# Optimization experiments

Measured on AMD Instinct MI355X. Metric: run time of the kernel, lower is better.

The kernel has to match this reference:

```python
import jax, jax.numpy as jnp
import numpy as np

N = 512          # octave output grid resolution per cube side
M = 256          # input octave resolution
FACTOR = 0.5     # 2 ** (-factor), factor = 1
EPS = 1e-12


def make_cube_faces(n):
    # two triangles per quad on each of the 6 n x n side grids
    idx = np.arange(n * n).reshape(n, n)
    a = idx[:-1, :-1].ravel(); b = idx[:-1, 1:].ravel()
    c = idx[1:, :-1].ravel(); d = idx[1:, 1:].ravel()
    tris = np.concatenate([np.stack([a, b, c], 1), np.stack([b, d, c], 1)], 0)
    faces = np.concatenate([tris + s * n * n for s in range(6)], 0)
    return jnp.asarray(faces, jnp.int32)  # [F, 3]


def to_stacked(t):
    # [1, 6*m*m, 3] -> [6, 3, m, m]
    m = int(round((t.shape[1] // 6) ** 0.5))
    return t.reshape(6, m, m, 3).transpose(0, 3, 1, 2)


def to_vertices(s):
    # [6, 3, m, m] -> [1, 6*m*m, 3]
    return s.transpose(0, 2, 3, 1).reshape(1, -1, 3)


def resize_bilinear_ac(t, n):
    # bilinear, align_corners=True, square input [.., m, m] -> [.., n, n]
    m = t.shape[-1]
    coords = jnp.linspace(0.0, m - 1.0, n)
    i0 = jnp.clip(jnp.floor(coords).astype(jnp.int32), 0, m - 1)
    i1 = jnp.minimum(i0 + 1, m - 1)
    w = (coords - i0).astype(t.dtype)
    t = t[..., i0, :] * (1.0 - w)[:, None] + t[..., i1, :] * w[:, None]
    t = t[..., :, i0] * (1.0 - w) + t[..., :, i1] * w
    return t


def compute_face_normals(vert, faces):
    v = vert[0]                                  # [V, 3]
    v0, v1, v2 = v[faces[:, 0]], v[faces[:, 1]], v[faces[:, 2]]
    fn = jnp.cross(v1 - v0, v2 - v0)             # [F, 3]
    nrm = jnp.linalg.norm(fn, axis=-1, keepdims=True)
    return fn / jnp.maximum(nrm, EPS)


def compute_vertex_normals(vert, faces, face_normals):
    V = vert.shape[1]
    flat_idx = faces.reshape(-1)                          # [3F] f0v0,f0v1,f0v2,...
    rep = jnp.repeat(face_normals, 3, axis=0)             # [3F, 3]
    acc = jax.ops.segment_sum(rep, flat_idx, num_segments=V)  # scatter-add
    nrm = jnp.linalg.norm(acc, axis=-1, keepdims=True)
    return (acc / jnp.maximum(nrm, EPS))[None]            # [1, V, 3]


def get_vertex_normals(vert, faces):
    fn = compute_face_normals(vert, faces)
    normals = compute_vertex_normals(vert, faces, fn)
    stacked = to_stacked(normals)                         # [6, 3, n, n]
    sign = jnp.array([-1.0, 1.0, 1.0, -1.0, -1.0, 1.0], stacked.dtype)
    stacked = stacked * sign[:, None, None, None]
    return to_vertices(stacked)


def setup_inputs() -> dict:
    key = jax.random.key(0)
    k1, k2 = jax.random.split(key)
    vrt = jax.random.normal(k1, (1, 6 * M * M, 3), jnp.float32)
    nrm = jax.random.normal(k2, (1, 6 * M * M, 3), jnp.float32)
    ps = jnp.zeros((6, 1, N, N), jnp.float32)   # nn.Parameter(zeros * noise)
    faces = make_cube_faces(N)
    return {"vrt": vrt, "nrm": nrm, "ps": ps, "faces": faces}


def reference(vrt, nrm, ps, faces):
    vrt_s = resize_bilinear_ac(to_stacked(vrt), N)                 # [6,3,n,n]
    nrm_mag = jnp.linalg.norm(resize_bilinear_ac(to_stacked(nrm), N),
                              axis=1, keepdims=True)               # [6,1,n,n]
    stacked = vrt_s + FACTOR * jax.nn.sigmoid(ps) * nrm_mag
    vert = to_vertices(stacked)                                    # [1, V, 3]
    normals = get_vertex_normals(vert, faces)
    return vert, faces, normals
```

## Files before the change

kernel.cpp:

```cpp
#include <hip/hip_runtime.h>
#include <math.h>

#define NSZ 512
#define MSZ 256
#define NPIX (6 * NSZ * NSZ)
#define NQu  261121u
#define NQ2u 522242u
#define NFACE 3133452
#define F3TOT 9400356
#define NFT12 783363
#define TS 32
#define HS 34
#define QS 33
#define NVB 1536
#define NFB ((NFT12 + 255) / 256)
#define GRID (NVB + NFB)

typedef __fp16 h2_t __attribute__((ext_vector_type(2)));

__device__ inline float fast_rcp(float x) {
    float r = __builtin_amdgcn_rcpf(x);
    return r * (2.0f - x * r);
}
__device__ inline float fast_rsqrt(float d) {
    float r = __builtin_amdgcn_rsqf(d);
    return r * (1.5f - 0.5f * d * r * r);
}
__device__ inline float fast_sigmoid(float x) {
    float e = __builtin_amdgcn_exp2f(-1.442695040888963f * x);
    return fast_rcp(1.0f + e);
}
__device__ inline float lerpf(float a, float b, float w) {
    return __builtin_fmaf(w, b - a, a);
}
__device__ inline unsigned pkh2(float x, float y) {
    h2_t h = __builtin_amdgcn_cvt_pkrtz(x, y);
    return __builtin_bit_cast(unsigned, h);
}
__device__ inline float2 uph2(unsigned u) {
    h2_t h = __builtin_bit_cast(h2_t, u);
    return make_float2((float)h.x, (float)h.y);
}
__device__ inline float uph_lo(unsigned u) {
    h2_t h = __builtin_bit_cast(h2_t, u);
    return (float)h.x;
}

__global__ __launch_bounds__(256, 8) void k_all(const float* __restrict__ vrt,
                                                const float* __restrict__ nrm,
                                                const float* __restrict__ ps,
                                                float* __restrict__ out0,
                                                float* __restrict__ out1,
                                                float* __restrict__ out2) {
    __shared__ unsigned svXY[HS * HS];
    __shared__ unsigned short svZ[HS * HS];
    __shared__ unsigned tnXY0[QS * QS];
    __shared__ unsigned tnXY1[QS * QS];
    __shared__ unsigned tnZZ [QS * QS];

    int blk = blockIdx.x;

    if (blk >= NVB) {
        int t = (blk - NVB) * 256 + threadIdx.x;
        if (t >= NFT12) return;
        unsigned tri = 4u * (unsigned)t;
        unsigned s   = tri / NQ2u;
        unsigned r1  = tri - s * NQ2u;
        unsigned ty  = (r1 >= NQu) ? 1u : 0u;
        unsigned qi  = r1 - ty * NQu;
        unsigned R   = qi / 511u;
        unsigned Q   = qi - R * 511u;

        unsigned a[4], tt[4];
        unsigned aq = Q, aR = R, aty = ty, as_ = s;
#pragma unroll
        for (int k = 0; k < 4; ++k) {
            a[k]  = (as_ << 18) + (aR << 9) + aq;
            tt[k] = aty;
            aq++;
            if (aq == 511u) {
                aq = 0u; aR++;
                if (aR == 511u) { aR = 0u; aty ^= 1u; if (aty == 0u) as_++; }
            }
        }
        float w[12];
#pragma unroll
        for (int k = 0; k < 4; ++k) {
            w[3*k + 0] = (float)(a[k] + (tt[k] ? 1u : 0u));
            w[3*k + 1] = (float)(a[k] + (tt[k] ? 513u : 1u));
            w[3*k + 2] = (float)(a[k] + 512u);
        }
        float4* o = (float4*)out1 + 3 * t;
        o[0] = make_float4(w[0], w[1], w[2],  w[3]);
        o[1] = make_float4(w[4], w[5], w[6],  w[7]);
        o[2] = make_float4(w[8], w[9], w[10], w[11]);
        return;
    }

    int f   = blk >> 8;
    int tl  = blk & 255;
    int tr  = (tl >> 4) * TS;
    int tq  = (tl & 15) * TS;
    int fbm = f * (MSZ * MSZ);
    int fbn = f * (NSZ * NSZ);

    const float scale = 255.0f / 511.0f;
    for (int p = threadIdx.x; p < HS * HS; p += 256) {
        int pr = p / HS, pq = p - pr * HS;
        int y = tr + pr - 1, x = tq + pq - 1;
        int yc = min(max(y, 0), NSZ - 1);
        int xc = min(max(x, 0), NSZ - 1);

        float cy = (float)yc * scale;
        float cx = (float)xc * scale;
        int iy0 = min((int)cy, MSZ - 1);
        int ix0 = min((int)cx, MSZ - 1);
        float wy = cy - (float)iy0;
        float wx = cx - (float)ix0;
        int   iya = min(iy0, MSZ - 2);
        int   ixa = min(ix0, MSZ - 2);
        float wya = (iy0 < MSZ - 1) ? wy : 1.0f;
        float wxa = (ix0 < MSZ - 1) ? wx : 1.0f;

        int g0 = (fbm + iya * MSZ + ixa) * 3;
        int g1 = g0 + MSZ * 3;

        float vx, vy, vz;
        {
            float a0 = vrt[g0], a1 = vrt[g0+1], a2 = vrt[g0+2];
            float a3 = vrt[g0+3], a4 = vrt[g0+4], a5 = vrt[g0+5];
            float b0 = vrt[g1], b1 = vrt[g1+1], b2 = vrt[g1+2];
            float b3 = vrt[g1+3], b4 = vrt[g1+4], b5 = vrt[g1+5];
            vx = lerpf(lerpf(a0, a3, wxa), lerpf(b0, b3, wxa), wya);
            vy = lerpf(lerpf(a1, a4, wxa), lerpf(b1, b4, wxa), wya);
            vz = lerpf(lerpf(a2, a5, wxa), lerpf(b2, b5, wxa), wya);
        }
        float nx, ny, nz;
        {
            float a0 = nrm[g0], a1 = nrm[g0+1], a2 = nrm[g0+2];
            float a3 = nrm[g0+3], a4 = nrm[g0+4], a5 = nrm[g0+5];
            float b0 = nrm[g1], b1 = nrm[g1+1], b2 = nrm[g1+2];
            float b3 = nrm[g1+3], b4 = nrm[g1+4], b5 = nrm[g1+5];
            nx = lerpf(lerpf(a0, a3, wxa), lerpf(b0, b3, wxa), wya);
            ny = lerpf(lerpf(a1, a4, wxa), lerpf(b1, b4, wxa), wya);
            nz = lerpf(lerpf(a2, a5, wxa), lerpf(b2, b5, wxa), wya);
        }

        float mag = __builtin_amdgcn_sqrtf(nx * nx + ny * ny + nz * nz);
        float sig = fast_sigmoid(ps[fbn + yc * NSZ + xc]);
        float add = 0.5f * sig * mag;
        float ox = vx + add, oy = vy + add, oz = vz + add;

        svXY[p] = pkh2(ox, oy);
        svZ[p]  = (unsigned short)(pkh2(oz, 0.0f) & 0xffffu);
        if (pr >= 1 && pr <= TS && pq >= 1 && pq <= TS) {
            int gi = (fbn + y * NSZ + x) * 3;
            out0[gi + 0] = ox;
            out0[gi + 1] = oy;
            out0[gi + 2] = oz;
        }
    }
    __syncthreads();

    for (int p = threadIdx.x; p < QS * QS; p += 256) {
        int Ri = p / QS, Qi = p - Ri * QS;
        int iA = Ri * HS + Qi;
        int iB = iA + 1;
        int iC = iA + HS;
        int iD = iC + 1;

        float2 Axy = uph2(svXY[iA]); float Az = uph_lo((unsigned)svZ[iA]);
        float2 Bxy = uph2(svXY[iB]); float Bz = uph_lo((unsigned)svZ[iB]);
        float2 Cxy = uph2(svXY[iC]); float Cz = uph_lo((unsigned)svZ[iC]);
        float2 Dxy = uph2(svXY[iD]); float Dz = uph_lo((unsigned)svZ[iD]);

        float n0x, n0y, n0z;
        {
            float e1x = Bxy.x - Axy.x, e1y = Bxy.y - Axy.y, e1z = Bz - Az;
            float e2x = Cxy.x - Axy.x, e2y = Cxy.y - Axy.y, e2z = Cz - Az;
            float cx = e1y * e2z - e1z * e2y;
            float cy = e1z * e2x - e1x * e2z;
            float cz = e1x * e2y - e1y * e2x;
            float d  = fmaxf(cx * cx + cy * cy + cz * cz, 1e-24f);
            float r  = fast_rsqrt(d);
            n0x = cx * r; n0y = cy * r; n0z = cz * r;
        }
        float n1x, n1y, n1z;
        {
            float e1x = Dxy.x - Bxy.x, e1y = Dxy.y - Bxy.y, e1z = Dz - Bz;
            float e2x = Cxy.x - Bxy.x, e2y = Cxy.y - Bxy.y, e2z = Cz - Bz;
            float cx = e1y * e2z - e1z * e2y;
            float cy = e1z * e2x - e1x * e2z;
            float cz = e1x * e2y - e1y * e2x;
            float d  = fmaxf(cx * cx + cy * cy + cz * cz, 1e-24f);
            float r  = fast_rsqrt(d);
            n1x = cx * r; n1y = cy * r; n1z = cz * r;
        }
        tnXY0[p] = pkh2(n0x, n0y);
        tnXY1[p] = pkh2(n1x, n1y);
        tnZZ [p] = pkh2(n0z, n1z);
    }
    __syncthreads();

    float sg = (f == 1 || f == 2 || f == 5) ? 1.0f : -1.0f;
    for (int p = threadIdx.x; p < TS * TS; p += 256) {
        int r = p >> 5, q = p & 31;
        int q00 = r * QS + q;
        int q01 = q00 + 1;
        int q10 = q00 + QS;
        int q11 = q10 + 1;

        float2 a0 = uph2(tnXY0[q11]);
        float2 a1 = uph2(tnXY0[q10]);
        float2 a2 = uph2(tnXY0[q01]);
        float2 b0 = uph2(tnXY1[q10]);
        float2 b1 = uph2(tnXY1[q00]);
        float2 b2 = uph2(tnXY1[q01]);
        float2 zA = uph2(tnZZ[q11]);
        float2 zB = uph2(tnZZ[q10]);
        float2 zC = uph2(tnZZ[q01]);
        float2 zD = uph2(tnZZ[q00]);

        float ax = a0.x + a1.x + a2.x + b0.x + b1.x + b2.x;
        float ay = a0.y + a1.y + a2.y + b0.y + b1.y + b2.y;
        float az = zA.x + zB.x + zC.x + zB.y + zD.y + zC.y;

        float d  = fmaxf(ax * ax + ay * ay + az * az, 1e-24f);
        float rs = fast_rsqrt(d) * sg;
        int gi = (fbn + (tr + r) * NSZ + (tq + q)) * 3;
        out2[gi + 0] = ax * rs;
        out2[gi + 1] = ay * rs;
        out2[gi + 2] = az * rs;
    }
}

extern "C" void kernel_launch(void* const* d_in, const int* in_sizes, int n_in,
                              void* d_out, int out_size, void* d_ws, size_t ws_size,
                              hipStream_t stream) {
    const float* vrt = (const float*)d_in[0];
    const float* nrm = (const float*)d_in[1];
    const float* ps  = (const float*)d_in[2];

    float* out0 = (float*)d_out;
    float* out1 = out0 + (size_t)NPIX * 3;
    float* out2 = out1 + (size_t)F3TOT;

    k_all<<<GRID, 256, 0, stream>>>(vrt, nrm, ps, out0, out1, out2);
}
```

Measured before the change: 26.84 us.

## Process four pixels per thread with float4 stores and packed-half normal sums

```diff
diff --git a/kernel.cpp b/kernel.cpp
--- a/kernel.cpp
+++ b/kernel.cpp
@@ -41,19 +41,18 @@
     h2_t h = __builtin_bit_cast(h2_t, u);
     return make_float2((float)h.x, (float)h.y);
 }
-__device__ inline float uph_lo(unsigned u) {
-    h2_t h = __builtin_bit_cast(h2_t, u);
-    return (float)h.x;
-}
-
-__global__ __launch_bounds__(256, 8) void k_all(const float* __restrict__ vrt,
-                                                const float* __restrict__ nrm,
-                                                const float* __restrict__ ps,
-                                                float* __restrict__ out0,
-                                                float* __restrict__ out1,
-                                                float* __restrict__ out2) {
-    __shared__ unsigned svXY[HS * HS];
-    __shared__ unsigned short svZ[HS * HS];
+__device__ inline unsigned pkadd(unsigned a, unsigned b) {
+    h2_t r = __builtin_bit_cast(h2_t, a) + __builtin_bit_cast(h2_t, b);
+    return __builtin_bit_cast(unsigned, r);
+}
+
+__global__ __launch_bounds__(256) void k_all(const float* __restrict__ vrt,
+                                             const float* __restrict__ nrm,
+                                             const float* __restrict__ ps,
+                                             float* __restrict__ out0,
+                                             float* __restrict__ out1,
+                                             float* __restrict__ out2) {
+    __shared__ float sv[HS * HS * 3];
     __shared__ unsigned tnXY0[QS * QS];
     __shared__ unsigned tnXY1[QS * QS];
     __shared__ unsigned tnZZ [QS * QS];
@@ -103,81 +102,131 @@
     int tq  = (tl & 15) * TS;
     int fbm = f * (MSZ * MSZ);
     int fbn = f * (NSZ * NSZ);
-
     const float scale = 255.0f / 511.0f;
-    for (int p = threadIdx.x; p < HS * HS; p += 256) {
-        int pr = p / HS, pq = p - pr * HS;
-        int y = tr + pr - 1, x = tq + pq - 1;
-        int yc = min(max(y, 0), NSZ - 1);
-        int xc = min(max(x, 0), NSZ - 1);
-
-        float cy = (float)yc * scale;
-        float cx = (float)xc * scale;
-        int iy0 = min((int)cy, MSZ - 1);
-        int ix0 = min((int)cx, MSZ - 1);
-        float wy = cy - (float)iy0;
-        float wx = cx - (float)ix0;
-        int   iya = min(iy0, MSZ - 2);
-        int   ixa = min(ix0, MSZ - 2);
-        float wya = (iy0 < MSZ - 1) ? wy : 1.0f;
-        float wxa = (ix0 < MSZ - 1) ? wx : 1.0f;
-
-        int g0 = (fbm + iya * MSZ + ixa) * 3;
-        int g1 = g0 + MSZ * 3;
-
-        float vx, vy, vz;
-        {
-            float a0 = vrt[g0], a1 = vrt[g0+1], a2 = vrt[g0+2];
-            float a3 = vrt[g0+3], a4 = vrt[g0+4], a5 = vrt[g0+5];
-            float b0 = vrt[g1], b1 = vrt[g1+1], b2 = vrt[g1+2];
-            float b3 = vrt[g1+3], b4 = vrt[g1+4], b5 = vrt[g1+5];
-            vx = lerpf(lerpf(a0, a3, wxa), lerpf(b0, b3, wxa), wya);
-            vy = lerpf(lerpf(a1, a4, wxa), lerpf(b1, b4, wxa), wya);
-            vz = lerpf(lerpf(a2, a5, wxa), lerpf(b2, b5, wxa), wya);
-        }
-        float nx, ny, nz;
-        {
-            float a0 = nrm[g0], a1 = nrm[g0+1], a2 = nrm[g0+2];
-            float a3 = nrm[g0+3], a4 = nrm[g0+4], a5 = nrm[g0+5];
-            float b0 = nrm[g1], b1 = nrm[g1+1], b2 = nrm[g1+2];
-            float b3 = nrm[g1+3], b4 = nrm[g1+4], b5 = nrm[g1+5];
-            nx = lerpf(lerpf(a0, a3, wxa), lerpf(b0, b3, wxa), wya);
-            ny = lerpf(lerpf(a1, a4, wxa), lerpf(b1, b4, wxa), wya);
-            nz = lerpf(lerpf(a2, a5, wxa), lerpf(b2, b5, wxa), wya);
-        }
-
-        float mag = __builtin_amdgcn_sqrtf(nx * nx + ny * ny + nz * nz);
-        float sig = fast_sigmoid(ps[fbn + yc * NSZ + xc]);
-        float add = 0.5f * sig * mag;
-        float ox = vx + add, oy = vy + add, oz = vz + add;
-
-        svXY[p] = pkh2(ox, oy);
-        svZ[p]  = (unsigned short)(pkh2(oz, 0.0f) & 0xffffu);
-        if (pr >= 1 && pr <= TS && pq >= 1 && pq <= TS) {
-            int gi = (fbn + y * NSZ + x) * 3;
-            out0[gi + 0] = ox;
-            out0[gi + 1] = oy;
-            out0[gi + 2] = oz;
+
+    for (int p = threadIdx.x; p < 340; p += 256) {
+        if (p < 272) {
+            int pr = p >> 3, j = p & 7;
+            int pq0 = 1 + 4 * j;
+            int y  = tr + pr - 1;
+            int yc = min(max(y, 0), NSZ - 1);
+            int xbase = tq + pq0 - 1;
+
+            float cy = (float)yc * scale;
+            int iy0 = min((int)cy, MSZ - 1);
+            float wy = cy - (float)iy0;
+            int   iya = min(iy0, MSZ - 2);
+            float wya = (iy0 < MSZ - 1) ? wy : 1.0f;
+
+            int ix0s[4]; float wxs[4];
+#pragma unroll
+            for (int i = 0; i < 4; ++i) {
+                float cx = (float)(xbase + i) * scale;
+                int ix0 = min((int)cx, MSZ - 1);
+                ix0s[i] = ix0;
+                wxs[i]  = (ix0 < MSZ - 1) ? (cx - (float)ix0) : 1.0f;
+            }
+            int c0 = min(min(ix0s[0], MSZ - 2), MSZ - 4);
+
+            int g0 = (fbm + iya * MSZ + c0) * 3;
+            int g1 = g0 + MSZ * 3;
+
+            float Yv[12], Yn[12];
+#pragma unroll
+            for (int c = 0; c < 12; ++c)
+                Yv[c] = lerpf(vrt[g0 + c], vrt[g1 + c], wya);
+#pragma unroll
+            for (int c = 0; c < 12; ++c)
+                Yn[c] = lerpf(nrm[g0 + c], nrm[g1 + c], wya);
+
+            float ov[12];
+#pragma unroll
+            for (int i = 0; i < 4; ++i) {
+                int li = min(ix0s[i], MSZ - 2) - c0;
+                int b  = 3 * li;
+                float wxa = wxs[i];
+                float vx = lerpf(Yv[b + 0], Yv[b + 3], wxa);
+                float vy = lerpf(Yv[b + 1], Yv[b + 4], wxa);
+                float vz = lerpf(Yv[b + 2], Yv[b + 5], wxa);
+                float nx = lerpf(Yn[b + 0], Yn[b + 3], wxa);
+                float ny = lerpf(Yn[b + 1], Yn[b + 4], wxa);
+                float nz = lerpf(Yn[b + 2], Yn[b + 5], wxa);
+                float mag = __builtin_amdgcn_sqrtf(nx * nx + ny * ny + nz * nz);
+                float sig = fast_sigmoid(ps[fbn + yc * NSZ + xbase + i]);
+                float add = 0.5f * sig * mag;
+                float ox = vx + add, oy = vy + add, oz = vz + add;
+                int sb = (pr * HS + pq0 + i) * 3;
+                sv[sb + 0] = ox; sv[sb + 1] = oy; sv[sb + 2] = oz;
+                ov[3 * i + 0] = ox; ov[3 * i + 1] = oy; ov[3 * i + 2] = oz;
+            }
+            if (pr >= 1 && pr <= TS) {
+                float4* o = (float4*)&out0[(size_t)(fbn + y * NSZ + xbase) * 3];
+                o[0] = make_float4(ov[0], ov[1], ov[2],  ov[3]);
+                o[1] = make_float4(ov[4], ov[5], ov[6],  ov[7]);
+                o[2] = make_float4(ov[8], ov[9], ov[10], ov[11]);
+            }
+        } else {
+            int e  = p - 272;
+            int pr = e >> 1;
+            int pq = (e & 1) ? (HS - 1) : 0;
+            int y = tr + pr - 1, x = tq + pq - 1;
+            int yc = min(max(y, 0), NSZ - 1);
+            int xc = min(max(x, 0), NSZ - 1);
+
+            float cy = (float)yc * scale;
+            float cx = (float)xc * scale;
+            int iy0 = min((int)cy, MSZ - 1);
+            int ix0 = min((int)cx, MSZ - 1);
+            float wy = cy - (float)iy0;
+            float wx = cx - (float)ix0;
+            int   iya = min(iy0, MSZ - 2);
+            int   ixa = min(ix0, MSZ - 2);
+            float wya = (iy0 < MSZ - 1) ? wy : 1.0f;
+            float wxa = (ix0 < MSZ - 1) ? wx : 1.0f;
+
+            int g0 = (fbm + iya * MSZ + ixa) * 3;
+            int g1 = g0 + MSZ * 3;
+
+            float vx, vy, vz, nx, ny, nz;
+            {
+                float a0 = vrt[g0], a1 = vrt[g0+1], a2 = vrt[g0+2];
+                float a3 = vrt[g0+3], a4 = vrt[g0+4], a5 = vrt[g0+5];
+                float b0 = vrt[g1], b1 = vrt[g1+1], b2 = vrt[g1+2];
+                float b3 = vrt[g1+3], b4 = vrt[g1+4], b5 = vrt[g1+5];
+                vx = lerpf(lerpf(a0, a3, wxa), lerpf(b0, b3, wxa), wya);
+                vy = lerpf(lerpf(a1, a4, wxa), lerpf(b1, b4, wxa), wya);
+                vz = lerpf(lerpf(a2, a5, wxa), lerpf(b2, b5, wxa), wya);
+            }
+            {
+                float a0 = nrm[g0], a1 = nrm[g0+1], a2 = nrm[g0+2];
+                float a3 = nrm[g0+3], a4 = nrm[g0+4], a5 = nrm[g0+5];
+                float b0 = nrm[g1], b1 = nrm[g1+1], b2 = nrm[g1+2];
+                float b3 = nrm[g1+3], b4 = nrm[g1+4], b5 = nrm[g1+5];
+                nx = lerpf(lerpf(a0, a3, wxa), lerpf(b0, b3, wxa), wya);
+                ny = lerpf(lerpf(a1, a4, wxa), lerpf(b1, b4, wxa), wya);
+                nz = lerpf(lerpf(a2, a5, wxa), lerpf(b2, b5, wxa), wya);
+            }
+            float mag = __builtin_amdgcn_sqrtf(nx * nx + ny * ny + nz * nz);
+            float sig = fast_sigmoid(ps[fbn + yc * NSZ + xc]);
+            float add = 0.5f * sig * mag;
+            int sb = (pr * HS + pq) * 3;
+            sv[sb + 0] = vx + add; sv[sb + 1] = vy + add; sv[sb + 2] = vz + add;
         }
     }
     __syncthreads();
 
     for (int p = threadIdx.x; p < QS * QS; p += 256) {
         int Ri = p / QS, Qi = p - Ri * QS;
-        int iA = Ri * HS + Qi;
-        int iB = iA + 1;
-        int iC = iA + HS;
-        int iD = iC + 1;
-
-        float2 Axy = uph2(svXY[iA]); float Az = uph_lo((unsigned)svZ[iA]);
-        float2 Bxy = uph2(svXY[iB]); float Bz = uph_lo((unsigned)svZ[iB]);
-        float2 Cxy = uph2(svXY[iC]); float Cz = uph_lo((unsigned)svZ[iC]);
-        float2 Dxy = uph2(svXY[iD]); float Dz = uph_lo((unsigned)svZ[iD]);
+        int base = (Ri * HS + Qi) * 3;
+        float Axx = sv[base + 0],        Axy = sv[base + 1],        Axz = sv[base + 2];
+        float Bxx = sv[base + 3],        Bxy = sv[base + 4],        Bxz = sv[base + 5];
+        float Cxx = sv[base + HS*3 + 0], Cxy = sv[base + HS*3 + 1], Cxz = sv[base + HS*3 + 2];
+        float Dxx = sv[base + HS*3 + 3], Dxy = sv[base + HS*3 + 4], Dxz = sv[base + HS*3 + 5];
 
         float n0x, n0y, n0z;
         {
-            float e1x = Bxy.x - Axy.x, e1y = Bxy.y - Axy.y, e1z = Bz - Az;
-            float e2x = Cxy.x - Axy.x, e2y = Cxy.y - Axy.y, e2z = Cz - Az;
+            float e1x = Bxx - Axx, e1y = Bxy - Axy, e1z = Bxz - Axz;
+            float e2x = Cxx - Axx, e2y = Cxy - Axy, e2z = Cxz - Axz;
             float cx = e1y * e2z - e1z * e2y;
             float cy = e1z * e2x - e1x * e2z;
             float cz = e1x * e2y - e1y * e2x;
@@ -187,8 +236,8 @@
         }
         float n1x, n1y, n1z;
         {
-            float e1x = Dxy.x - Bxy.x, e1y = Dxy.y - Bxy.y, e1z = Dz - Bz;
-            float e2x = Cxy.x - Bxy.x, e2y = Cxy.y - Bxy.y, e2z = Cz - Bz;
+            float e1x = Dxx - Bxx, e1y = Dxy - Bxy, e1z = Dxz - Bxz;
+            float e2x = Cxx - Bxx, e2y = Cxy - Bxy, e2z = Cxz - Bxz;
             float cx = e1y * e2z - e1z * e2y;
             float cy = e1z * e2x - e1x * e2z;
             float cz = e1x * e2y - e1y * e2x;
@@ -203,34 +252,45 @@
     __syncthreads();
 
     float sg = (f == 1 || f == 2 || f == 5) ? 1.0f : -1.0f;
-    for (int p = threadIdx.x; p < TS * TS; p += 256) {
-        int r = p >> 5, q = p & 31;
-        int q00 = r * QS + q;
-        int q01 = q00 + 1;
-        int q10 = q00 + QS;
-        int q11 = q10 + 1;
-
-        float2 a0 = uph2(tnXY0[q11]);
-        float2 a1 = uph2(tnXY0[q10]);
-        float2 a2 = uph2(tnXY0[q01]);
-        float2 b0 = uph2(tnXY1[q10]);
-        float2 b1 = uph2(tnXY1[q00]);
-        float2 b2 = uph2(tnXY1[q01]);
-        float2 zA = uph2(tnZZ[q11]);
-        float2 zB = uph2(tnZZ[q10]);
-        float2 zC = uph2(tnZZ[q01]);
-        float2 zD = uph2(tnZZ[q00]);
-
-        float ax = a0.x + a1.x + a2.x + b0.x + b1.x + b2.x;
-        float ay = a0.y + a1.y + a2.y + b0.y + b1.y + b2.y;
-        float az = zA.x + zB.x + zC.x + zB.y + zD.y + zC.y;
-
-        float d  = fmaxf(ax * ax + ay * ay + az * az, 1e-24f);
-        float rs = fast_rsqrt(d) * sg;
-        int gi = (fbn + (tr + r) * NSZ + (tq + q)) * 3;
-        out2[gi + 0] = ax * rs;
-        out2[gi + 1] = ay * rs;
-        out2[gi + 2] = az * rs;
+    {
+        int r  = threadIdx.x >> 3;
+        int q0 = (threadIdx.x & 7) * 4;
+        int b0 = r * QS + q0;
+        int b1 = b0 + QS;
+
+        unsigned t0r0[5], t0r1[5], t1r0[5], t1r1[5], zr0[5], zr1[5];
+#pragma unroll
+        for (int c = 0; c < 5; ++c) {
+            t0r0[c] = tnXY0[b0 + c];
+            t0r1[c] = tnXY0[b1 + c];
+            t1r0[c] = tnXY1[b0 + c];
+            t1r1[c] = tnXY1[b1 + c];
+            zr0[c]  = tnZZ [b0 + c];
+            zr1[c]  = tnZZ [b1 + c];
+        }
+
+        float ov[12];
+#pragma unroll
+        for (int i = 0; i < 4; ++i) {
+            unsigned axy = pkadd(pkadd(pkadd(t0r1[i+1], t0r1[i]),
+                                       pkadd(t0r0[i+1], t1r1[i])),
+                                 pkadd(t1r0[i],  t1r0[i+1]));
+            float2 xy = uph2(axy);
+            unsigned S = pkadd(zr1[i], zr0[i+1]);
+            float2 s1 = uph2(pkadd(S, zr1[i+1]));
+            float2 s2 = uph2(pkadd(S, zr0[i]));
+            float az = s1.x + s2.y;
+
+            float d  = fmaxf(xy.x * xy.x + xy.y * xy.y + az * az, 1e-24f);
+            float rs = fast_rsqrt(d) * sg;
+            ov[3*i + 0] = xy.x * rs;
+            ov[3*i + 1] = xy.y * rs;
+            ov[3*i + 2] = az  * rs;
+        }
+        float4* o = (float4*)&out2[(size_t)(fbn + (tr + r) * NSZ + tq + q0) * 3];
+        o[0] = make_float4(ov[0], ov[1], ov[2],  ov[3]);
+        o[1] = make_float4(ov[4], ov[5], ov[6],  ov[7]);
+        o[2] = make_float4(ov[8], ov[9], ov[10], ov[11]);
     }
 }
 
```

After: 36.34 us. 35.4% more time.

## Interleave face-index blocks with vertex tiles and store fp32 vertices in LDS

Applied to the files above, without the earlier changes.

```diff
diff --git a/kernel.cpp b/kernel.cpp
--- a/kernel.cpp
+++ b/kernel.cpp
@@ -13,8 +13,7 @@
 #define HS 34
 #define QS 33
 #define NVB 1536
-#define NFB ((NFT12 + 255) / 256)
-#define GRID (NVB + NFB)
+#define GRID (NVB * 3)
 
 typedef __fp16 h2_t __attribute__((ext_vector_type(2)));
 
@@ -41,27 +40,24 @@
     h2_t h = __builtin_bit_cast(h2_t, u);
     return make_float2((float)h.x, (float)h.y);
 }
-__device__ inline float uph_lo(unsigned u) {
-    h2_t h = __builtin_bit_cast(h2_t, u);
-    return (float)h.x;
-}
-
-__global__ __launch_bounds__(256, 8) void k_all(const float* __restrict__ vrt,
-                                                const float* __restrict__ nrm,
-                                                const float* __restrict__ ps,
-                                                float* __restrict__ out0,
-                                                float* __restrict__ out1,
-                                                float* __restrict__ out2) {
-    __shared__ unsigned svXY[HS * HS];
-    __shared__ unsigned short svZ[HS * HS];
+
+__global__ __launch_bounds__(256) void k_all(const float* __restrict__ vrt,
+                                             const float* __restrict__ nrm,
+                                             const float* __restrict__ ps,
+                                             float* __restrict__ out0,
+                                             float* __restrict__ out1,
+                                             float* __restrict__ out2) {
+    __shared__ float sv[HS * HS * 3];
     __shared__ unsigned tnXY0[QS * QS];
     __shared__ unsigned tnXY1[QS * QS];
     __shared__ unsigned tnZZ [QS * QS];
 
     int blk = blockIdx.x;
-
-    if (blk >= NVB) {
-        int t = (blk - NVB) * 256 + threadIdx.x;
+    int grp = blk / 3;
+    int pos = blk - grp * 3;
+
+    if (pos != 0) {
+        int t = (grp * 2 + (pos - 1)) * 256 + threadIdx.x;
         if (t >= NFT12) return;
         unsigned tri = 4u * (unsigned)t;
         unsigned s   = tri / NQ2u;
@@ -97,8 +93,8 @@
         return;
     }
 
-    int f   = blk >> 8;
-    int tl  = blk & 255;
+    int f   = grp >> 8;
+    int tl  = grp & 255;
     int tr  = (tl >> 4) * TS;
     int tq  = (tl & 15) * TS;
     int fbm = f * (MSZ * MSZ);
@@ -151,8 +147,9 @@
         float add = 0.5f * sig * mag;
         float ox = vx + add, oy = vy + add, oz = vz + add;
 
-        svXY[p] = pkh2(ox, oy);
-        svZ[p]  = (unsigned short)(pkh2(oz, 0.0f) & 0xffffu);
+        sv[p * 3 + 0] = ox;
+        sv[p * 3 + 1] = oy;
+        sv[p * 3 + 2] = oz;
         if (pr >= 1 && pr <= TS && pq >= 1 && pq <= TS) {
             int gi = (fbn + y * NSZ + x) * 3;
             out0[gi + 0] = ox;
@@ -164,20 +161,16 @@
 
     for (int p = threadIdx.x; p < QS * QS; p += 256) {
         int Ri = p / QS, Qi = p - Ri * QS;
-        int iA = Ri * HS + Qi;
-        int iB = iA + 1;
-        int iC = iA + HS;
-        int iD = iC + 1;
-
-        float2 Axy = uph2(svXY[iA]); float Az = uph_lo((unsigned)svZ[iA]);
-        float2 Bxy = uph2(svXY[iB]); float Bz = uph_lo((unsigned)svZ[iB]);
-        float2 Cxy = uph2(svXY[iC]); float Cz = uph_lo((unsigned)svZ[iC]);
-        float2 Dxy = uph2(svXY[iD]); float Dz = uph_lo((unsigned)svZ[iD]);
+        int base = (Ri * HS + Qi) * 3;
+        float Axx = sv[base + 0],        Axy = sv[base + 1],        Axz = sv[base + 2];
+        float Bxx = sv[base + 3],        Bxy = sv[base + 4],        Bxz = sv[base + 5];
+        float Cxx = sv[base + HS*3 + 0], Cxy = sv[base + HS*3 + 1], Cxz = sv[base + HS*3 + 2];
+        float Dxx = sv[base + HS*3 + 3], Dxy = sv[base + HS*3 + 4], Dxz = sv[base + HS*3 + 5];
 
         float n0x, n0y, n0z;
         {
-            float e1x = Bxy.x - Axy.x, e1y = Bxy.y - Axy.y, e1z = Bz - Az;
-            float e2x = Cxy.x - Axy.x, e2y = Cxy.y - Axy.y, e2z = Cz - Az;
+            float e1x = Bxx - Axx, e1y = Bxy - Axy, e1z = Bxz - Axz;
+            float e2x = Cxx - Axx, e2y = Cxy - Axy, e2z = Cxz - Axz;
             float cx = e1y * e2z - e1z * e2y;
             float cy = e1z * e2x - e1x * e2z;
             float cz = e1x * e2y - e1y * e2x;
@@ -187,8 +180,8 @@
         }
         float n1x, n1y, n1z;
         {
-            float e1x = Dxy.x - Bxy.x, e1y = Dxy.y - Bxy.y, e1z = Dz - Bz;
-            float e2x = Cxy.x - Bxy.x, e2y = Cxy.y - Bxy.y, e2z = Cz - Bz;
+            float e1x = Dxx - Bxx, e1y = Dxy - Bxy, e1z = Dxz - Bxz;
+            float e2x = Cxx - Bxx, e2y = Cxy - Bxy, e2z = Cxz - Bxz;
             float cx = e1y * e2z - e1z * e2y;
             float cy = e1z * e2x - e1x * e2z;
             float cz = e1x * e2y - e1y * e2x;
```

Result: slower. 28.94 us (+7.8%).
